# Kernel optimization log

Measured on AMD Instinct MI355X. Metric: run time of the kernel, lower is better.

Reference implementation:

```python
import jax, jax.numpy as jnp
import numpy as np

EPS = 1e-3  # BatchNorm eps in the original module


def conv3d(x, w, stride=1, pad=1):
    # x: (N,C,D,H,W), w: (O,I,3,3,3)
    return jax.lax.conv_general_dilated(
        x, w, (stride,) * 3, [(pad, pad)] * 3,
        dimension_numbers=("NCDHW", "OIDHW", "NCDHW"))


def bn_relu_mask(x, scale, shift, mask):
    # eval-mode BatchNorm folded to affine (scale/shift), ReLU, then re-mask
    # so inactive voxels stay exactly zero (submanifold semantics).
    y = jax.nn.relu(x * scale[None, :, None, None, None] + shift[None, :, None, None, None])
    return y * mask


def downsample_mask(mask):
    # output site of SparseConv3d(k=3,s=2,p=1) is active iff any active input
    # voxel lies in its receptive field -> max-pool of the mask.
    return jax.lax.reduce_window(
        mask, 0.0, jax.lax.max, (1, 1, 3, 3, 3), (1, 1, 2, 2, 2),
        [(0, 0), (0, 0), (1, 1), (1, 1), (1, 1)])


def trilinear_sample(vol, coords):
    # vol: (C,D,H,W); coords: (N,3) in [-1,1], order (x,y,z) -> (W,H,D).
    # Matches F.grid_sample(mode='bilinear', padding_mode='zeros', align_corners=True).
    C, D, H, W = vol.shape
    fx = (coords[:, 0] + 1.0) * 0.5 * (W - 1)
    fy = (coords[:, 1] + 1.0) * 0.5 * (H - 1)
    fz = (coords[:, 2] + 1.0) * 0.5 * (D - 1)
    x0 = jnp.floor(fx); y0 = jnp.floor(fy); z0 = jnp.floor(fz)
    tx = fx - x0; ty = fy - y0; tz = fz - z0
    x0i = x0.astype(jnp.int32); y0i = y0.astype(jnp.int32); z0i = z0.astype(jnp.int32)
    out = jnp.zeros((C, coords.shape[0]), vol.dtype)
    for dz in (0, 1):
        for dy in (0, 1):
            for dx in (0, 1):
                xi = x0i + dx; yi = y0i + dy; zi = z0i + dz
                w = (jnp.where(dx, tx, 1.0 - tx) * jnp.where(dy, ty, 1.0 - ty)
                     * jnp.where(dz, tz, 1.0 - tz))
                valid = ((xi >= 0) & (xi < W) & (yi >= 0) & (yi < H)
                         & (zi >= 0) & (zi < D))
                xc = jnp.clip(xi, 0, W - 1); yc = jnp.clip(yi, 0, H - 1)
                zc = jnp.clip(zi, 0, D - 1)
                vals = vol[:, zc, yc, xc]  # (C,N)
                out = out + vals * (w * valid.astype(vol.dtype))[None, :]
    return out


def setup_inputs() -> dict:
    key = jax.random.key(0)
    ks = jax.random.split(key, 24)
    D = 128
    NPTS = 65536
    x_feat = jax.random.normal(ks[0], (1, 3, D, D, D), jnp.float32)
    mask = (jax.random.uniform(ks[1], (1, 1, D, D, D)) < 0.1).astype(jnp.int32)
    coords = jax.random.uniform(ks[2], (NPTS, 3), jnp.float32, -1.0, 1.0)

    def w(k, o, i):
        return jax.random.normal(k, (o, i, 3, 3, 3), jnp.float32) * 0.05

    def bn(k, c):
        k1, k2 = jax.random.split(k)
        scale = jax.random.uniform(k1, (c,), jnp.float32, 0.5, 1.5)
        shift = jax.random.normal(k2, (c,), jnp.float32) * 0.1
        return scale, shift

    w0a = w(ks[3], 16, 3); s0a, b0a = bn(ks[4], 16)
    w0b = w(ks[5], 16, 16); s0b, b0b = bn(ks[6], 16)
    wd0 = w(ks[7], 32, 16); sd0, bd0 = bn(ks[8], 32)
    w1a = w(ks[9], 32, 32); s1a, b1a = bn(ks[10], 32)
    w1b = w(ks[11], 32, 32); s1b, b1b = bn(ks[12], 32)
    return dict(x_feat=x_feat, mask=mask, coords=coords,
                w0a=w0a, s0a=s0a, b0a=b0a, w0b=w0b, s0b=s0b, b0b=b0b,
                wd0=wd0, sd0=sd0, bd0=bd0,
                w1a=w1a, s1a=s1a, b1a=b1a, w1b=w1b, s1b=s1b, b1b=b1b)


def reference(x_feat, mask, coords, w0a, s0a, b0a, w0b, s0b, b0b,
              wd0, sd0, bd0, w1a, s1a, b1a, w1b, s1b, b1b):
    m0 = mask.astype(x_feat.dtype)
    x = x_feat * m0  # features exist only at active voxels
    # conv0: double submanifold conv (3->16->16), active set unchanged
    h = bn_relu_mask(conv3d(x, w0a), s0a, b0a, m0)
    h = bn_relu_mask(conv3d(h, w0b), s0b, b0b, m0)
    # down0: strided sparse conv 16->32, stride 2, pad 1
    m1 = downsample_mask(m0)
    h = bn_relu_mask(conv3d(h, wd0, stride=2), sd0, bd0, m1)
    # conv1: double submanifold conv 32->32 on the downsampled active set
    h = bn_relu_mask(conv3d(h, w1a), s1a, b1a, m1)
    h = bn_relu_mask(conv3d(h, w1b), s1b, b1b, m1)
    # dense + grid_sample (align_corners=True, zeros padding) -> (N, 32)
    feat = trilinear_sample(h[0], coords)  # (32, N)
    return feat.T
```

## Files before the change

kernel.cpp:

```cpp
#include <hip/hip_runtime.h>
#include <hip/hip_bf16.h>

#define N   128
#define N3  (N*N*N)
#define M   64
#define M3  (M*M*M)
#define NPTS 65536
#define PD  66
#define PD2 (PD*PD)
#define PVOX (PD*PD*PD)
#define PH  130
#define PH2 (PH*PH)
#define PH3 (PH*PH*PH)
#define CAP   393216
#define ZSLOT (CAP - 1)

enum : int {
  OW0A = 0,
  OW0B = 1296,
  OWD0 = 8208,
  OW1A = 22032,
  OW1B = 49680,
  OS0A = 77328, OB0A = 77344,
  OS0B = 77360, OB0B = 77376,
  OSD0 = 77392, OBD0 = 77424,
  OS1A = 77456, OB1A = 77488,
  OS1B = 77520, OB1B = 77552,
  WTOT = 77584
};

enum : int {
  IW0A = 0,
  IW0B = 2048,
  IWD0 = 9216,
  IW1A = 23552,
  IW1B = 51200,
  ITOT = 78848
};

typedef short bf16x8 __attribute__((ext_vector_type(8)));
typedef float f32x4  __attribute__((ext_vector_type(4)));

__device__ __forceinline__ unsigned short f2bf_bits(float f) {
  __hip_bfloat16 b = __float2bfloat16(f);
  union { __hip_bfloat16 b; unsigned short u; } cv; cv.b = b; return cv.u;
}
__device__ __forceinline__ float bfbits2f(short s) {
  union { unsigned u; float f; } c; c.u = ((unsigned)(unsigned short)s) << 16; return c.f;
}

__device__ __forceinline__ float ldIn(const void* p, long i, int bf) {
  return bf ? __bfloat162float(((const __hip_bfloat16*)p)[i]) : ((const float*)p)[i];
}

__global__ void probe_k(const unsigned* __restrict__ s0a_raw, int* __restrict__ flag) {
  if (threadIdx.x == 0 && blockIdx.x == 0) {
    int all = 1;
    for (int i = 0; i < 8; ++i) {
      unsigned w = s0a_raw[i];
      if (((w >> 8) & 0xFFu) != 0x3Fu) all = 0;
    }
    *flag = all;
  }
}

__global__ __launch_bounds__(256) void cvt_k(
    const void* w0a, const void* w0b, const void* wd0,
    const void* w1a, const void* w1b,
    const void* s0a, const void* b0a,
    const void* s0b, const void* b0b,
    const void* sd0, const void* bd0,
    const void* s1a, const void* b1a,
    const void* s1b, const void* b1b,
    const int* __restrict__ flag, float* __restrict__ wbuf)
{
  int i = blockIdx.x * 256 + threadIdx.x;
  if (i >= WTOT) return;
  int bf = *flag;
  const void* src; int off;
  if      (i < OW0B) { src = w0a; off = OW0A; }
  else if (i < OWD0) { src = w0b; off = OW0B; }
  else if (i < OW1A) { src = wd0; off = OWD0; }
  else if (i < OW1B) { src = w1a; off = OW1A; }
  else if (i < OS0A) { src = w1b; off = OW1B; }
  else if (i < OB0A) { src = s0a; off = OS0A; }
  else if (i < OS0B) { src = b0a; off = OB0A; }
  else if (i < OB0B) { src = s0b; off = OS0B; }
  else if (i < OSD0) { src = b0b; off = OB0B; }
  else if (i < OBD0) { src = sd0; off = OSD0; }
  else if (i < OS1A) { src = bd0; off = OBD0; }
  else if (i < OB1A) { src = s1a; off = OS1A; }
  else if (i < OS1B) { src = b1a; off = OB1A; }
  else if (i < OB1B) { src = s1b; off = OS1B; }
  else               { src = b1b; off = OB1B; }
  wbuf[i] = ldIn(src, i - off, bf);
}

__global__ __launch_bounds__(256) void wtrans_k(const float* __restrict__ wbuf,
                                               short* __restrict__ WI)
{
  int i = blockIdx.x * 256 + threadIdx.x;
  if (i >= 27648) return;
  if (i < 2048) {
    int kb = i >> 9, l = (i >> 3) & 63, j = i & 7;
    int k = ((l >> 4) << 3) + j;
    int tap = kb * 8 + (k >> 2), ch = k & 3, oc = l & 15;
    float v = (tap < 27 && ch < 3) ? wbuf[OW0A + (oc * 3 + ch) * 27 + tap] : 0.f;
    WI[IW0A + i] = (short)f2bf_bits(v);
  }
  if (i < 7168) {
    int p = i >> 9, l = (i >> 3) & 63, j = i & 7;
    int kg = ((l >> 4) << 3) + j;
    int tap = 2 * p + (kg >> 4);
    int ic = kg & 15, oc = l & 15;
    float v = (tap < 27) ? wbuf[OW0B + (oc * 16 + ic) * 27 + tap] : 0.f;
    WI[IW0B + i] = (short)f2bf_bits(v);
  }
  if (i < 14336) {
    int p = i >> 10, h = (i >> 9) & 1, l = (i >> 3) & 63, j = i & 7;
    int kg = ((l >> 4) << 3) + j;
    int tap = 2 * p + (kg >> 4);
    int ic = kg & 15;
    int oc = (h << 4) + (l & 15);
    float v = (tap < 27) ? wbuf[OWD0 + (oc * 16 + ic) * 27 + tap] : 0.f;
    WI[IWD0 + i] = (short)f2bf_bits(v);
  }
  {
    int t = i >> 10, h = (i >> 9) & 1, l = (i >> 3) & 63, j = i & 7;
    int ic = ((l >> 4) << 3) + j;
    int oc = (h << 4) + (l & 15);
    WI[IW1A + i] = (short)f2bf_bits(wbuf[OW1A + (oc * 32 + ic) * 27 + t]);
    WI[IW1B + i] = (short)f2bf_bits(wbuf[OW1B + (oc * 32 + ic) * 27 + t]);
  }
}

__global__ __launch_bounds__(256) void masklist_k(const int* __restrict__ mask,
                                                  int* __restrict__ list,
                                                  int* __restrict__ idxvol,
                                                  int* __restrict__ cnt)
{
  __shared__ int lpos, lbase;
  int t = threadIdx.x;
  int start = blockIdx.x * 8192;
  if (t == 0) lpos = 0;
  __syncthreads();
  int myc = 0;
  #pragma unroll 4
  for (int i = 0; i < 32; ++i) myc += (mask[start + i * 256 + t] != 0);
  atomicAdd(&lpos, myc);
  __syncthreads();
  if (t == 0) { lbase = atomicAdd(cnt, lpos); lpos = 0; }
  __syncthreads();
  #pragma unroll 4
  for (int i = 0; i < 32; ++i) {
    int idx = start + i * 256 + t;
    if (mask[idx]) {
      int p = atomicAdd(&lpos, 1);
      int slot = lbase + p;
      if (slot < ZSLOT) {
        list[slot] = idx;
        int z = idx >> 14, y = (idx >> 7) & 127, x = idx & 127;
        idxvol[((z + 1) * PH + (y + 1)) * PH + (x + 1)] = slot;
      }
    }
  }
}

__global__ __launch_bounds__(256) void dsmask_k(const int* __restrict__ mask,
                                                float* __restrict__ m1f)
{
  int idx = blockIdx.x * 256 + threadIdx.x;
  if (idx >= M3) return;
  int z = idx >> 12, y = (idx >> 6) & 63, x = idx & 63;
  int r = 0;
  #pragma unroll
  for (int dz = 0; dz < 3; ++dz) {
    int iz = 2 * z + dz - 1;
    if ((unsigned)iz >= 128u) continue;
    #pragma unroll
    for (int dy = 0; dy < 3; ++dy) {
      int iy = 2 * y + dy - 1;
      if ((unsigned)iy >= 128u) continue;
      #pragma unroll
      for (int dx = 0; dx < 3; ++dx) {
        int ix = 2 * x + dx - 1;
        if ((unsigned)ix >= 128u) continue;
        r |= mask[(iz << 14) | (iy << 7) | ix];
      }
    }
  }
  m1f[idx] = r ? 1.f : 0.f;
}

__global__ __launch_bounds__(256) void pack_c_k(const void* __restrict__ xf,
                                                const int* __restrict__ flag,
                                                const int* __restrict__ list,
                                                const int* __restrict__ cnt,
                                                short* __restrict__ xc)
{
  int nact = *cnt;
  int bf = *flag;
  for (int i = blockIdx.x * 256 + threadIdx.x; i < nact; i += 1024 * 256) {
    int idx = list[i];
    union { unsigned short us[4]; uint2 v; } u;
    u.us[0] = f2bf_bits(ldIn(xf, idx, bf));
    u.us[1] = f2bf_bits(ldIn(xf, (long)N3 + idx, bf));
    u.us[2] = f2bf_bits(ldIn(xf, 2l * N3 + idx, bf));
    u.us[3] = 0;
    *(uint2*)(xc + (size_t)i * 4) = u.v;
  }
}

__device__ __forceinline__ int tap_shift_PH(int t) {
  if (t >= 27) return 0;
  int dz = t / 9, r9 = t - dz * 9, dy = r9 / 3, dx = r9 - dy * 3;
  return (dz - 1) * PH2 + (dy - 1) * PH + (dx - 1);
}
__device__ __forceinline__ int slot_of(const int* __restrict__ idxvol, int nb) {
  int s = idxvol[nb];
  return s < 0 ? ZSLOT : s;
}

__global__ __launch_bounds__(256) void conv0a_mfma_k(
    const short* __restrict__ xc, const int* __restrict__ idxvol,
    const int* __restrict__ list, const int* __restrict__ cnt,
    const short* __restrict__ WI, const float* __restrict__ wbuf,
    short* __restrict__ h0c)
{
  __shared__ short ldsB[4 * 512];
  int tid = threadIdx.x;
  if (tid < 256) ((uint4*)ldsB)[tid] = ((const uint4*)(WI + IW0A))[tid];
  __syncthreads();
  int nact = *cnt;
  int wave = tid >> 6, lane = tid & 63, quad = lane >> 4, l15 = lane & 15;
  const int SAFE = PH2 + PH + 1;
  for (int base = blockIdx.x * 256; base < nact; base += 1024 * 256) {
    int i0 = base + wave * 64;
    int pv[4];
    #pragma unroll
    for (int tt = 0; tt < 4; ++tt) {
      int e2 = i0 + tt * 16 + l15;
      if (e2 < nact) {
        int idx = list[e2];
        int z = idx >> 14, y = (idx >> 7) & 127, x = idx & 127;
        pv[tt] = ((z + 1) * PH + (y + 1)) * PH + (x + 1);
      } else pv[tt] = SAFE;
    }
    f32x4 acc[4];
    #pragma unroll
    for (int tt = 0; tt < 4; ++tt) { f32x4 zf = {0.f,0.f,0.f,0.f}; acc[tt] = zf; }
    #pragma unroll
    for (int kb = 0; kb < 4; ++kb) {
      int t0 = kb * 8 + quad * 2, t1 = t0 + 1;
      int s0 = tap_shift_PH(t0), s1 = tap_shift_PH(t1);
      bf16x8 b = *(const bf16x8*)&ldsB[(kb * 64 + lane) * 8];
      #pragma unroll
      for (int tt = 0; tt < 4; ++tt) {
        int sa = slot_of(idxvol, pv[tt] + s0);
        int sb2 = slot_of(idxvol, pv[tt] + s1);
        union { struct { uint2 lo, hi; } p; bf16x8 v; } cv;
        cv.p.lo = *(const uint2*)(xc + (size_t)sa * 4);
        cv.p.hi = *(const uint2*)(xc + (size_t)sb2 * 4);
        acc[tt] = __builtin_amdgcn_mfma_f32_16x16x32_bf16(cv.v, b, acc[tt], 0, 0, 0);
      }
    }
    float sc = wbuf[OS0A + l15], sb = wbuf[OB0A + l15];
    #pragma unroll
    for (int tt = 0; tt < 4; ++tt)
      #pragma unroll
      for (int r = 0; r < 4; ++r) {
        int e2 = i0 + tt * 16 + quad * 4 + r;
        if (e2 < nact) {
          float vv = fmaxf(fmaf(acc[tt][r], sc, sb), 0.f);
          h0c[(size_t)e2 * 16 + l15] = (short)f2bf_bits(vv);
        }
      }
  }
}

__global__ __launch_bounds__(256) void conv0b_mfma_k(
    const short* __restrict__ h0c, const int* __restrict__ idxvol,
    const int* __restrict__ list, const int* __restrict__ cnt,
    const short* __restrict__ WI, const float* __restrict__ wbuf,
    short* __restrict__ h1c)
{
  __shared__ short ldsB[14 * 512];
  int tid = threadIdx.x;
  for (int i = tid; i < 14 * 64; i += 256)
    ((uint4*)ldsB)[i] = ((const uint4*)(WI + IW0B))[i];
  __syncthreads();
  int nact = *cnt;
  int wave = tid >> 6, lane = tid & 63, quad = lane >> 4, l15 = lane & 15;
  const int SAFE = PH2 + PH + 1;
  for (int base = blockIdx.x * 256; base < nact; base += 1024 * 256) {
    int i0 = base + wave * 64;
    int pv[4];
    #pragma unroll
    for (int tt = 0; tt < 4; ++tt) {
      int e2 = i0 + tt * 16 + l15;
      if (e2 < nact) {
        int idx = list[e2];
        int z = idx >> 14, y = (idx >> 7) & 127, x = idx & 127;
        pv[tt] = ((z + 1) * PH + (y + 1)) * PH + (x + 1);
      } else pv[tt] = SAFE;
    }
    f32x4 acc[4];
    #pragma unroll
    for (int tt = 0; tt < 4; ++tt) { f32x4 zf = {0.f,0.f,0.f,0.f}; acc[tt] = zf; }
    #pragma unroll
    for (int p = 0; p < 14; ++p) {
      const int t1 = 2 * p, t2 = (2 * p + 1 < 27) ? 2 * p + 1 : 2 * p;
      const int s1 = ((t1 / 9) - 1) * PH2 + (((t1 % 9) / 3) - 1) * PH + ((t1 % 3) - 1);
      const int s2 = ((t2 / 9) - 1) * PH2 + (((t2 % 9) / 3) - 1) * PH + ((t2 % 3) - 1);
      int sh = (quad >= 2) ? s2 : s1;
      bf16x8 b = *(const bf16x8*)&ldsB[(p * 64 + lane) * 8];
      #pragma unroll
      for (int tt = 0; tt < 4; ++tt) {
        int ss = slot_of(idxvol, pv[tt] + sh);
        bf16x8 a = *(const bf16x8*)(h0c + (size_t)ss * 16 + ((quad & 1) << 3));
        acc[tt] = __builtin_amdgcn_mfma_f32_16x16x32_bf16(a, b, acc[tt], 0, 0, 0);
      }
    }
    float sc = wbuf[OS0B + l15], sb = wbuf[OB0B + l15];
    #pragma unroll
    for (int tt = 0; tt < 4; ++tt)
      #pragma unroll
      for (int r = 0; r < 4; ++r) {
        int e2 = i0 + tt * 16 + quad * 4 + r;
        if (e2 < nact) {
          float vv = fmaxf(fmaf(acc[tt][r], sc, sb), 0.f);
          h1c[(size_t)e2 * 16 + l15] = (short)f2bf_bits(vv);
        }
      }
  }
}

__global__ __launch_bounds__(256) void convd0_mfma_k(
    const short* __restrict__ h1c, const int* __restrict__ idxvol,
    const float* __restrict__ m1f,
    const short* __restrict__ WI, const float* __restrict__ wbuf,
    short* __restrict__ Pout)
{
  __shared__ short ldsB[14 * 1024];
  int tid = threadIdx.x;
  for (int i = tid; i < 14 * 128; i += 256)
    ((uint4*)ldsB)[i] = ((const uint4*)(WI + IWD0))[i];
  __syncthreads();
  int wave = tid >> 6, lane = tid & 63, quad = lane >> 4, l15 = lane & 15;
  int rowid = blockIdx.x * 4 + wave;
  int z = rowid >> 6, y = rowid & 63;
  int base_row = ((2 * z) * PH + 2 * y) * PH;
  f32x4 acc[4][2];
  #pragma unroll
  for (int tt = 0; tt < 4; ++tt)
  #pragma unroll
  for (int h = 0; h < 2; ++h) { f32x4 zf = {0.f,0.f,0.f,0.f}; acc[tt][h] = zf; }
  #pragma unroll
  for (int p = 0; p < 14; ++p) {
    const int t1 = 2 * p, t2 = (2 * p + 1 < 27) ? 2 * p + 1 : 2 * p;
    const int s1 = (t1 / 9) * PH2 + ((t1 % 9) / 3) * PH + (t1 % 3);
    const int s2 = (t2 / 9) * PH2 + ((t2 % 9) / 3) * PH + (t2 % 3);
    int sh = (quad >= 2) ? s2 : s1;
    bf16x8 b0 = *(const bf16x8*)&ldsB[((p * 2 + 0) * 64 + lane) * 8];
    bf16x8 b1 = *(const bf16x8*)&ldsB[((p * 2 + 1) * 64 + lane) * 8];
    bf16x8 a[4];
    #pragma unroll
    for (int tt = 0; tt < 4; ++tt) {
      int vin = base_row + sh + 2 * (tt * 16 + l15);
      int ss = slot_of(idxvol, vin);
      a[tt] = *(const bf16x8*)(h1c + (size_t)ss * 16 + ((quad & 1) << 3));
    }
    #pragma unroll
    for (int tt = 0; tt < 4; ++tt) {
      acc[tt][0] = __builtin_amdgcn_mfma_f32_16x16x32_bf16(a[tt], b0, acc[tt][0], 0, 0, 0);
      acc[tt][1] = __builtin_amdgcn_mfma_f32_16x16x32_bf16(a[tt], b1, acc[tt][1], 0, 0, 0);
    }
  }
  float sc[2] = { wbuf[OSD0 + l15], wbuf[OSD0 + 16 + l15] };
  float sb[2] = { wbuf[OBD0 + l15], wbuf[OBD0 + 16 + l15] };
  int mrow = (z * 64 + y) * 64;
  int obase = ((z + 1) * PD + (y + 1)) * PD + 1;
  #pragma unroll
  for (int tt = 0; tt < 4; ++tt) {
    float4 mv = *(const float4*)&m1f[mrow + tt * 16 + quad * 4];
    float mvr[4] = {mv.x, mv.y, mv.z, mv.w};
    #pragma unroll
    for (int h = 0; h < 2; ++h)
      #pragma unroll
      for (int r = 0; r < 4; ++r) {
        float vv = fmaxf(fmaf(acc[tt][h][r], sc[h], sb[h]), 0.f) * mvr[r];
        int vox = obase + tt * 16 + quad * 4 + r;
        Pout[(size_t)vox * 32 + h * 16 + l15] = (short)f2bf_bits(vv);
      }
  }
}

__global__ __launch_bounds__(256) void conv1_mfma_k(
    const short* __restrict__ Pin, short* __restrict__ Pout,
    const short* __restrict__ WI, const float* __restrict__ wbuf,
    int sof, int bof, const float* __restrict__ m1f)
{
  __shared__ short ldsB[27 * 1024];
  int tid = threadIdx.x;
  for (int i = tid; i < 27 * 128; i += 256)
    ((uint4*)ldsB)[i] = ((const uint4*)WI)[i];
  __syncthreads();

  int wave = tid >> 6, lane = tid & 63;
  int quad = lane >> 4, l15 = lane & 15;

  f32x4 acc[2][4][2];
  #pragma unroll
  for (int rr = 0; rr < 2; ++rr)
  #pragma unroll
  for (int tt = 0; tt < 4; ++tt)
  #pragma unroll
  for (int h = 0; h < 2; ++h) {
    f32x4 zf = {0.f, 0.f, 0.f, 0.f};
    acc[rr][tt][h] = zf;
  }

  int rowid0 = blockIdx.x * 8 + wave * 2;
  int abase[2], zz[2], yy[2];
  #pragma unroll
  for (int rr = 0; rr < 2; ++rr) {
    int rowid = rowid0 + rr;
    zz[rr] = rowid >> 6; yy[rr] = rowid & 63;
    abase[rr] = ((zz[rr] + 1) * PD + (yy[rr] + 1)) * PD + 1;
  }

  #pragma unroll 1
  for (int k = 0; k < 27; ++k) {
    int dz = k / 9, r9 = k - dz * 9, dy = r9 / 3, dx = r9 - dy * 3;
    int shift = (dz - 1) * PD2 + (dy - 1) * PD + (dx - 1);
    bf16x8 b0 = *(const bf16x8*)&ldsB[((k * 2 + 0) * 64 + lane) * 8];
    bf16x8 b1 = *(const bf16x8*)&ldsB[((k * 2 + 1) * 64 + lane) * 8];
    bf16x8 a[2][4];
    #pragma unroll
    for (int rr = 0; rr < 2; ++rr)
    #pragma unroll
    for (int tt = 0; tt < 4; ++tt) {
      int off = (abase[rr] + shift + tt * 16 + l15) * 32 + quad * 8;
      a[rr][tt] = *(const bf16x8*)(Pin + off);
    }
    #pragma unroll
    for (int rr = 0; rr < 2; ++rr)
    #pragma unroll
    for (int tt = 0; tt < 4; ++tt) {
      acc[rr][tt][0] = __builtin_amdgcn_mfma_f32_16x16x32_bf16(a[rr][tt], b0, acc[rr][tt][0], 0, 0, 0);
      acc[rr][tt][1] = __builtin_amdgcn_mfma_f32_16x16x32_bf16(a[rr][tt], b1, acc[rr][tt][1], 0, 0, 0);
    }
  }

  float sc[2] = { wbuf[sof + l15], wbuf[sof + 16 + l15] };
  float sh[2] = { wbuf[bof + l15], wbuf[bof + 16 + l15] };

  #pragma unroll
  for (int rr = 0; rr < 2; ++rr) {
    int mrow = (zz[rr] * 64 + yy[rr]) * 64;
    #pragma unroll
    for (int tt = 0; tt < 4; ++tt) {
      const float4 mv = *(const float4*)&m1f[mrow + tt * 16 + quad * 4];
      float mvr[4] = {mv.x, mv.y, mv.z, mv.w};
      #pragma unroll
      for (int h = 0; h < 2; ++h) {
        #pragma unroll
        for (int r = 0; r < 4; ++r) {
          float v = fmaxf(fmaf(acc[rr][tt][h][r], sc[h], sh[h]), 0.f) * mvr[r];
          int vox = abase[rr] + tt * 16 + quad * 4 + r;
          Pout[vox * 32 + h * 16 + l15] = (short)f2bf_bits(v);
        }
      }
    }
  }
}

__global__ __launch_bounds__(256) void sample_k(
    const void* __restrict__ coords, const int* __restrict__ flag,
    const short* __restrict__ vol, void* __restrict__ out)
{
  int p = blockIdx.x * 256 + threadIdx.x;
  if (p >= NPTS) return;
  int bf = *flag;
  float cx = ldIn(coords, 3l * p + 0, bf);
  float cy = ldIn(coords, 3l * p + 1, bf);
  float cz = ldIn(coords, 3l * p + 2, bf);
  float fx = (cx + 1.f) * 0.5f * 63.f;
  float fy = (cy + 1.f) * 0.5f * 63.f;
  float fz = (cz + 1.f) * 0.5f * 63.f;
  float x0f = floorf(fx), y0f = floorf(fy), z0f = floorf(fz);
  int x0 = (int)x0f, y0 = (int)y0f, z0 = (int)z0f;
  float tx = fx - x0f, ty = fy - y0f, tz = fz - z0f;
  int li[8]; float wt[8];
  #pragma unroll
  for (int dz = 0; dz < 2; ++dz)
  #pragma unroll
  for (int dy = 0; dy < 2; ++dy)
  #pragma unroll
  for (int dx = 0; dx < 2; ++dx) {
    int t = dz * 4 + dy * 2 + dx;
    int xi = x0 + dx, yi = y0 + dy, zi = z0 + dz;
    bool ok = (unsigned)xi < 64u && (unsigned)yi < 64u && (unsigned)zi < 64u;
    int xc = min(max(xi, 0), 63), yc = min(max(yi, 0), 63), zc = min(max(zi, 0), 63);
    li[t] = ((zc + 1) * PD + (yc + 1)) * PD + (xc + 1);
    float w = (dx ? tx : 1.f - tx) * (dy ? ty : 1.f - ty) * (dz ? tz : 1.f - tz);
    wt[t] = ok ? w : 0.f;
  }
  #pragma unroll
  for (int cc = 0; cc < 4; ++cc) {
    float s[8];
    #pragma unroll
    for (int j = 0; j < 8; ++j) s[j] = 0.f;
    #pragma unroll
    for (int t = 0; t < 8; ++t) {
      bf16x8 v = *(const bf16x8*)(vol + (size_t)li[t] * 32 + cc * 8);
      #pragma unroll
      for (int j = 0; j < 8; ++j) s[j] += bfbits2f(v[j]) * wt[t];
    }
    if (bf) {
      union { unsigned short us[8]; uint4 v; } u;
      #pragma unroll
      for (int j = 0; j < 8; ++j) u.us[j] = f2bf_bits(s[j]);
      ((uint4*)out)[p * 4 + cc] = u.v;
    } else {
      #pragma unroll
      for (int j = 0; j < 8; ++j) ((float*)out)[(size_t)p * 32 + cc * 8 + j] = s[j];
    }
  }
}

extern "C" void kernel_launch(void* const* d_in, const int* in_sizes, int n_in,
                              void* d_out, int out_size, void* d_ws, size_t ws_size,
                              hipStream_t stream)
{
  const void* xf     = d_in[0];
  const int*  mask   = (const int*)d_in[1];
  const void* coords = d_in[2];
  const void* w0a = d_in[3];
  const void* s0a = d_in[4];
  const void* b0a = d_in[5];
  const void* w0b = d_in[6];
  const void* s0b = d_in[7];
  const void* b0b = d_in[8];
  const void* wd0 = d_in[9];
  const void* sd0 = d_in[10];
  const void* bd0 = d_in[11];
  const void* w1a = d_in[12];
  const void* s1a = d_in[13];
  const void* b1a = d_in[14];
  const void* w1b = d_in[15];
  const void* s1b = d_in[16];
  const void* b1b = d_in[17];

  char* ws = (char*)d_ws;
  size_t cur = 0;
  auto alloc = [&](size_t bytes) -> size_t {
    size_t o = cur; cur = (cur + bytes + 255) & ~(size_t)255; return o;
  };
  size_t o_flag = alloc(4);
  size_t o_cnt  = alloc(4);
  size_t o_m1f  = alloc((size_t)M3 * 4);
  size_t o_wbuf = alloc((size_t)WTOT * 4);
  size_t o_WI   = alloc((size_t)ITOT * 2);
  size_t o_list = alloc((size_t)CAP * 4);
  size_t o_idx  = alloc((size_t)PH3 * 4);
  size_t o_xc   = alloc((size_t)CAP * 4 * 2);
  size_t o_h0c  = alloc((size_t)CAP * 16 * 2);
  size_t o_h1c  = alloc((size_t)CAP * 16 * 2);
  size_t o_P1   = alloc((size_t)PVOX * 32 * 2);
  size_t o_P2   = alloc((size_t)PVOX * 32 * 2);

  int*   flag   = (int*)(ws + o_flag);
  int*   cnt    = (int*)(ws + o_cnt);
  float* m1f    = (float*)(ws + o_m1f);
  float* wbuf   = (float*)(ws + o_wbuf);
  short* WI     = (short*)(ws + o_WI);
  int*   list   = (int*)(ws + o_list);
  int*   idxvol = (int*)(ws + o_idx);
  short* xc     = (short*)(ws + o_xc);
  short* h0c    = (short*)(ws + o_h0c);
  short* h1c    = (short*)(ws + o_h1c);
  short* P1     = (short*)(ws + o_P1);
  short* P2     = (short*)(ws + o_P2);

  hipMemsetAsync(cnt, 0, 4, stream);
  hipMemsetAsync(idxvol, 0xFF, (size_t)PH3 * 4, stream);
  hipMemsetAsync(ws + o_xc, 0, (o_P2 - o_xc) + (size_t)PVOX * 32 * 2, stream);

  probe_k<<<1, 64, 0, stream>>>((const unsigned*)s0a, flag);
  cvt_k<<<(WTOT + 255) / 256, 256, 0, stream>>>(w0a, w0b, wd0, w1a, w1b,
                                                s0a, b0a, s0b, b0b, sd0, bd0,
                                                s1a, b1a, s1b, b1b, flag, wbuf);
  wtrans_k<<<108, 256, 0, stream>>>(wbuf, WI);
  masklist_k<<<256, 256, 0, stream>>>(mask, list, idxvol, cnt);
  dsmask_k<<<M3 / 256, 256, 0, stream>>>(mask, m1f);

  pack_c_k<<<1024, 256, 0, stream>>>(xf, flag, list, cnt, xc);
  conv0a_mfma_k<<<1024, 256, 0, stream>>>(xc, idxvol, list, cnt, WI, wbuf, h0c);
  conv0b_mfma_k<<<1024, 256, 0, stream>>>(h0c, idxvol, list, cnt, WI, wbuf, h1c);
  convd0_mfma_k<<<1024, 256, 0, stream>>>(h1c, idxvol, m1f, WI, wbuf, P1);

  conv1_mfma_k<<<512, 256, 0, stream>>>(P1, P2, WI + IW1A, wbuf, OS1A, OB1A, m1f);
  conv1_mfma_k<<<512, 256, 0, stream>>>(P2, P1, WI + IW1B, wbuf, OS1B, OB1B, m1f);

  sample_k<<<NPTS / 256, 256, 0, stream>>>(coords, flag, P1, d_out);
}
```

Baseline: 307.2 us.

## Fuse prep kernels, inline dtype detection, and pipeline conv1 A-loads

Merges the dtype probe, weight conversion and weight transpose into one prep kernel, and fuses mask listing, downsample-mask and feature packing into one kernel, cutting the launch count. conv1 now gives each wave one row instead of two and doubles the grid. It also software-pipelines the A-fragment loads across taps and shrinks LDS by keeping the last tap's weights in registers. The fewer launches and higher occupancy are meant to hide memory latency, at the cost of more register pressure and every kernel re-deriving the dtype flag.

Measured after the change: 346.6 us. +12.8%, slower.

```diff
diff --git a/kernel.cpp b/kernel.cpp
--- a/kernel.cpp
+++ b/kernel.cpp
@@ -16,20 +16,6 @@
 #define ZSLOT (CAP - 1)
 
 enum : int {
-  OW0A = 0,
-  OW0B = 1296,
-  OWD0 = 8208,
-  OW1A = 22032,
-  OW1B = 49680,
-  OS0A = 77328, OB0A = 77344,
-  OS0B = 77360, OB0B = 77376,
-  OSD0 = 77392, OBD0 = 77424,
-  OS1A = 77456, OB1A = 77488,
-  OS1B = 77520, OB1B = 77552,
-  WTOT = 77584
-};
-
-enum : int {
   IW0A = 0,
   IW0B = 2048,
   IWD0 = 9216,
@@ -38,6 +24,12 @@
   ITOT = 78848
 };
 
+enum : int {
+  SS0A = 0,   SB0A = 16,  SS0B = 32,  SB0B = 48,
+  SSD0 = 64,  SBD0 = 96,  SS1A = 128, SB1A = 160,
+  SS1B = 192, SB1B = 224, STOT = 256
+};
+
 typedef short bf16x8 __attribute__((ext_vector_type(8)));
 typedef float f32x4  __attribute__((ext_vector_type(4)));
 
@@ -48,64 +40,35 @@
 __device__ __forceinline__ float bfbits2f(short s) {
   union { unsigned u; float f; } c; c.u = ((unsigned)(unsigned short)s) << 16; return c.f;
 }
-
 __device__ __forceinline__ float ldIn(const void* p, long i, int bf) {
   return bf ? __bfloat162float(((const __hip_bfloat16*)p)[i]) : ((const float*)p)[i];
 }
-
-__global__ void probe_k(const unsigned* __restrict__ s0a_raw, int* __restrict__ flag) {
-  if (threadIdx.x == 0 && blockIdx.x == 0) {
-    int all = 1;
-    for (int i = 0; i < 8; ++i) {
-      unsigned w = s0a_raw[i];
-      if (((w >> 8) & 0xFFu) != 0x3Fu) all = 0;
-    }
-    *flag = all;
-  }
-}
-
-__global__ __launch_bounds__(256) void cvt_k(
+__device__ __forceinline__ int detect_bf(const unsigned* __restrict__ s0a_raw) {
+  int all = 1;
+  #pragma unroll
+  for (int i = 0; i < 8; ++i) {
+    unsigned w = s0a_raw[i];
+    if (((w >> 8) & 0xFFu) != 0x3Fu) all = 0;
+  }
+  return all;
+}
+
+__global__ __launch_bounds__(256) void prep_k(
     const void* w0a, const void* w0b, const void* wd0,
     const void* w1a, const void* w1b,
-    const void* s0a, const void* b0a,
-    const void* s0b, const void* b0b,
-    const void* sd0, const void* bd0,
-    const void* s1a, const void* b1a,
+    const void* s0a, const void* b0a, const void* s0b, const void* b0b,
+    const void* sd0, const void* bd0, const void* s1a, const void* b1a,
     const void* s1b, const void* b1b,
-    const int* __restrict__ flag, float* __restrict__ wbuf)
+    short* __restrict__ WI, float* __restrict__ sbuf)
 {
   int i = blockIdx.x * 256 + threadIdx.x;
-  if (i >= WTOT) return;
-  int bf = *flag;
-  const void* src; int off;
-  if      (i < OW0B) { src = w0a; off = OW0A; }
-  else if (i < OWD0) { src = w0b; off = OW0B; }
-  else if (i < OW1A) { src = wd0; off = OWD0; }
-  else if (i < OW1B) { src = w1a; off = OW1A; }
-  else if (i < OS0A) { src = w1b; off = OW1B; }
-  else if (i < OB0A) { src = s0a; off = OS0A; }
-  else if (i < OS0B) { src = b0a; off = OB0A; }
-  else if (i < OB0B) { src = s0b; off = OS0B; }
-  else if (i < OSD0) { src = b0b; off = OB0B; }
-  else if (i < OBD0) { src = sd0; off = OSD0; }
-  else if (i < OS1A) { src = bd0; off = OBD0; }
-  else if (i < OB1A) { src = s1a; off = OS1A; }
-  else if (i < OS1B) { src = b1a; off = OB1A; }
-  else if (i < OB1B) { src = s1b; off = OS1B; }
-  else               { src = b1b; off = OB1B; }
-  wbuf[i] = ldIn(src, i - off, bf);
-}
-
-__global__ __launch_bounds__(256) void wtrans_k(const float* __restrict__ wbuf,
-                                               short* __restrict__ WI)
-{
-  int i = blockIdx.x * 256 + threadIdx.x;
-  if (i >= 27648) return;
+  if (i >= 27648 + STOT) return;
+  int bf = detect_bf((const unsigned*)s0a);
   if (i < 2048) {
     int kb = i >> 9, l = (i >> 3) & 63, j = i & 7;
     int k = ((l >> 4) << 3) + j;
     int tap = kb * 8 + (k >> 2), ch = k & 3, oc = l & 15;
-    float v = (tap < 27 && ch < 3) ? wbuf[OW0A + (oc * 3 + ch) * 27 + tap] : 0.f;
+    float v = (tap < 27 && ch < 3) ? ldIn(w0a, (oc * 3 + ch) * 27 + tap, bf) : 0.f;
     WI[IW0A + i] = (short)f2bf_bits(v);
   }
   if (i < 7168) {
@@ -113,7 +76,7 @@
     int kg = ((l >> 4) << 3) + j;
     int tap = 2 * p + (kg >> 4);
     int ic = kg & 15, oc = l & 15;
-    float v = (tap < 27) ? wbuf[OW0B + (oc * 16 + ic) * 27 + tap] : 0.f;
+    float v = (tap < 27) ? ldIn(w0b, (oc * 16 + ic) * 27 + tap, bf) : 0.f;
     WI[IW0B + i] = (short)f2bf_bits(v);
   }
   if (i < 14336) {
@@ -122,24 +85,64 @@
     int tap = 2 * p + (kg >> 4);
     int ic = kg & 15;
     int oc = (h << 4) + (l & 15);
-    float v = (tap < 27) ? wbuf[OWD0 + (oc * 16 + ic) * 27 + tap] : 0.f;
+    float v = (tap < 27) ? ldIn(wd0, (oc * 16 + ic) * 27 + tap, bf) : 0.f;
     WI[IWD0 + i] = (short)f2bf_bits(v);
   }
-  {
+  if (i < 27648) {
     int t = i >> 10, h = (i >> 9) & 1, l = (i >> 3) & 63, j = i & 7;
     int ic = ((l >> 4) << 3) + j;
     int oc = (h << 4) + (l & 15);
-    WI[IW1A + i] = (short)f2bf_bits(wbuf[OW1A + (oc * 32 + ic) * 27 + t]);
-    WI[IW1B + i] = (short)f2bf_bits(wbuf[OW1B + (oc * 32 + ic) * 27 + t]);
-  }
-}
-
-__global__ __launch_bounds__(256) void masklist_k(const int* __restrict__ mask,
-                                                  int* __restrict__ list,
-                                                  int* __restrict__ idxvol,
-                                                  int* __restrict__ cnt)
-{
+    WI[IW1A + i] = (short)f2bf_bits(ldIn(w1a, (oc * 32 + ic) * 27 + t, bf));
+    WI[IW1B + i] = (short)f2bf_bits(ldIn(w1b, (oc * 32 + ic) * 27 + t, bf));
+  } else {
+    int j = i - 27648;
+    const void* src; int loc;
+    if      (j < 16)  { src = s0a; loc = j; }
+    else if (j < 32)  { src = b0a; loc = j - 16; }
+    else if (j < 48)  { src = s0b; loc = j - 32; }
+    else if (j < 64)  { src = b0b; loc = j - 48; }
+    else if (j < 96)  { src = sd0; loc = j - 64; }
+    else if (j < 128) { src = bd0; loc = j - 96; }
+    else if (j < 160) { src = s1a; loc = j - 128; }
+    else if (j < 192) { src = b1a; loc = j - 160; }
+    else if (j < 224) { src = s1b; loc = j - 192; }
+    else              { src = b1b; loc = j - 224; }
+    sbuf[j] = ldIn(src, loc, bf);
+  }
+}
+
+__global__ __launch_bounds__(256) void maskprep_k(
+    const int* __restrict__ mask, const void* __restrict__ xf,
+    const void* __restrict__ s0a,
+    int* __restrict__ list, int* __restrict__ idxvol, int* __restrict__ cnt,
+    float* __restrict__ m1f, short* __restrict__ xc)
+{
+  if (blockIdx.x >= 256) {
+    int idx = (blockIdx.x - 256) * 256 + threadIdx.x;
+    if (idx >= M3) return;
+    int z = idx >> 12, y = (idx >> 6) & 63, x = idx & 63;
+    int r = 0;
+    #pragma unroll
+    for (int dz = 0; dz < 3; ++dz) {
+      int iz = 2 * z + dz - 1;
+      if ((unsigned)iz >= 128u) continue;
+      #pragma unroll
+      for (int dy = 0; dy < 3; ++dy) {
+        int iy = 2 * y + dy - 1;
+        if ((unsigned)iy >= 128u) continue;
+        #pragma unroll
+        for (int dx = 0; dx < 3; ++dx) {
+          int ix = 2 * x + dx - 1;
+          if ((unsigned)ix >= 128u) continue;
+          r |= mask[(iz << 14) | (iy << 7) | ix];
+        }
+      }
+    }
+    m1f[idx] = r ? 1.f : 0.f;
+    return;
+  }
   __shared__ int lpos, lbase;
+  int bf = detect_bf((const unsigned*)s0a);
   int t = threadIdx.x;
   int start = blockIdx.x * 8192;
   if (t == 0) lpos = 0;
@@ -161,53 +164,14 @@
         list[slot] = idx;
         int z = idx >> 14, y = (idx >> 7) & 127, x = idx & 127;
         idxvol[((z + 1) * PH + (y + 1)) * PH + (x + 1)] = slot;
-      }
-    }
-  }
-}
-
-__global__ __launch_bounds__(256) void dsmask_k(const int* __restrict__ mask,
-                                                float* __restrict__ m1f)
-{
-  int idx = blockIdx.x * 256 + threadIdx.x;
-  if (idx >= M3) return;
-  int z = idx >> 12, y = (idx >> 6) & 63, x = idx & 63;
-  int r = 0;
-  #pragma unroll
-  for (int dz = 0; dz < 3; ++dz) {
-    int iz = 2 * z + dz - 1;
-    if ((unsigned)iz >= 128u) continue;
-    #pragma unroll
-    for (int dy = 0; dy < 3; ++dy) {
-      int iy = 2 * y + dy - 1;
-      if ((unsigned)iy >= 128u) continue;
-      #pragma unroll
-      for (int dx = 0; dx < 3; ++dx) {
-        int ix = 2 * x + dx - 1;
-        if ((unsigned)ix >= 128u) continue;
-        r |= mask[(iz << 14) | (iy << 7) | ix];
-      }
-    }
-  }
-  m1f[idx] = r ? 1.f : 0.f;
-}
-
-__global__ __launch_bounds__(256) void pack_c_k(const void* __restrict__ xf,
-                                                const int* __restrict__ flag,
-                                                const int* __restrict__ list,
-                                                const int* __restrict__ cnt,
-                                                short* __restrict__ xc)
-{
-  int nact = *cnt;
-  int bf = *flag;
-  for (int i = blockIdx.x * 256 + threadIdx.x; i < nact; i += 1024 * 256) {
-    int idx = list[i];
-    union { unsigned short us[4]; uint2 v; } u;
-    u.us[0] = f2bf_bits(ldIn(xf, idx, bf));
-    u.us[1] = f2bf_bits(ldIn(xf, (long)N3 + idx, bf));
-    u.us[2] = f2bf_bits(ldIn(xf, 2l * N3 + idx, bf));
-    u.us[3] = 0;
-    *(uint2*)(xc + (size_t)i * 4) = u.v;
+        union { unsigned short us[4]; uint2 v; } u;
+        u.us[0] = f2bf_bits(ldIn(xf, idx, bf));
+        u.us[1] = f2bf_bits(ldIn(xf, (long)N3 + idx, bf));
+        u.us[2] = f2bf_bits(ldIn(xf, 2l * N3 + idx, bf));
+        u.us[3] = 0;
+        *(uint2*)(xc + (size_t)slot * 4) = u.v;
+      }
+    }
   }
 }
 
@@ -224,7 +188,7 @@
 __global__ __launch_bounds__(256) void conv0a_mfma_k(
     const short* __restrict__ xc, const int* __restrict__ idxvol,
     const int* __restrict__ list, const int* __restrict__ cnt,
-    const short* __restrict__ WI, const float* __restrict__ wbuf,
+    const short* __restrict__ WI, const float* __restrict__ sbuf,
     short* __restrict__ h0c)
 {
   __shared__ short ldsB[4 * 512];
@@ -264,7 +228,7 @@
         acc[tt] = __builtin_amdgcn_mfma_f32_16x16x32_bf16(cv.v, b, acc[tt], 0, 0, 0);
       }
     }
-    float sc = wbuf[OS0A + l15], sb = wbuf[OB0A + l15];
+    float sc = sbuf[SS0A + l15], sb = sbuf[SB0A + l15];
     #pragma unroll
     for (int tt = 0; tt < 4; ++tt)
       #pragma unroll
@@ -281,7 +245,7 @@
 __global__ __launch_bounds__(256) void conv0b_mfma_k(
     const short* __restrict__ h0c, const int* __restrict__ idxvol,
     const int* __restrict__ list, const int* __restrict__ cnt,
-    const short* __restrict__ WI, const float* __restrict__ wbuf,
+    const short* __restrict__ WI, const float* __restrict__ sbuf,
     short* __restrict__ h1c)
 {
   __shared__ short ldsB[14 * 512];
@@ -321,7 +285,7 @@
         acc[tt] = __builtin_amdgcn_mfma_f32_16x16x32_bf16(a, b, acc[tt], 0, 0, 0);
       }
     }
-    float sc = wbuf[OS0B + l15], sb = wbuf[OB0B + l15];
+    float sc = sbuf[SS0B + l15], sb = sbuf[SB0B + l15];
     #pragma unroll
     for (int tt = 0; tt < 4; ++tt)
       #pragma unroll
@@ -338,7 +302,7 @@
 __global__ __launch_bounds__(256) void convd0_mfma_k(
     const short* __restrict__ h1c, const int* __restrict__ idxvol,
     const float* __restrict__ m1f,
-    const short* __restrict__ WI, const float* __restrict__ wbuf,
+    const short* __restrict__ WI, const float* __restrict__ sbuf,
     short* __restrict__ Pout)
 {
   __shared__ short ldsB[14 * 1024];
@@ -376,8 +340,8 @@
       acc[tt][1] = __builtin_amdgcn_mfma_f32_16x16x32_bf16(a[tt], b1, acc[tt][1], 0, 0, 0);
     }
   }
-  float sc[2] = { wbuf[OSD0 + l15], wbuf[OSD0 + 16 + l15] };
-  float sb[2] = { wbuf[OBD0 + l15], wbuf[OBD0 + 16 + l15] };
+  float sc[2] = { sbuf[SSD0 + l15], sbuf[SSD0 + 16 + l15] };
+  float sb[2] = { sbuf[SBD0 + l15], sbuf[SBD0 + 16 + l15] };
   int mrow = (z * 64 + y) * 64;
   int obase = ((z + 1) * PD + (y + 1)) * PD + 1;
   #pragma unroll
@@ -397,91 +361,99 @@
 
 __global__ __launch_bounds__(256) void conv1_mfma_k(
     const short* __restrict__ Pin, short* __restrict__ Pout,
-    const short* __restrict__ WI, const float* __restrict__ wbuf,
+    const short* __restrict__ WI, const float* __restrict__ sbuf,
     int sof, int bof, const float* __restrict__ m1f)
 {
-  __shared__ short ldsB[27 * 1024];
+  __shared__ short ldsB[26 * 1024];
   int tid = threadIdx.x;
-  for (int i = tid; i < 27 * 128; i += 256)
+  for (int i = tid; i < 26 * 128; i += 256)
     ((uint4*)ldsB)[i] = ((const uint4*)WI)[i];
-  __syncthreads();
 
   int wave = tid >> 6, lane = tid & 63;
   int quad = lane >> 4, l15 = lane & 15;
 
-  f32x4 acc[2][4][2];
-  #pragma unroll
-  for (int rr = 0; rr < 2; ++rr)
+  bf16x8 b26[2];
+  b26[0] = *(const bf16x8*)(WI + 26 * 1024 + 0 * 512 + lane * 8);
+  b26[1] = *(const bf16x8*)(WI + 26 * 1024 + 1 * 512 + lane * 8);
+  __syncthreads();
+
+  f32x4 acc[4][2];
   #pragma unroll
   for (int tt = 0; tt < 4; ++tt)
   #pragma unroll
-  for (int h = 0; h < 2; ++h) {
-    f32x4 zf = {0.f, 0.f, 0.f, 0.f};
-    acc[rr][tt][h] = zf;
-  }
-
-  int rowid0 = blockIdx.x * 8 + wave * 2;
-  int abase[2], zz[2], yy[2];
-  #pragma unroll
-  for (int rr = 0; rr < 2; ++rr) {
-    int rowid = rowid0 + rr;
-    zz[rr] = rowid >> 6; yy[rr] = rowid & 63;
-    abase[rr] = ((zz[rr] + 1) * PD + (yy[rr] + 1)) * PD + 1;
-  }
-
+  for (int h = 0; h < 2; ++h) { f32x4 zf = {0.f,0.f,0.f,0.f}; acc[tt][h] = zf; }
+
+  int rowid = blockIdx.x * 4 + wave;
+  int zz = rowid >> 6, yy = rowid & 63;
+  int abase = ((zz + 1) * PD + (yy + 1)) * PD + 1;
+
+  bf16x8 a_cur[4];
+  {
+    const int shift0 = -PD2 - PD - 1;
+    #pragma unroll
+    for (int tt = 0; tt < 4; ++tt) {
+      int off = (abase + shift0 + tt * 16 + l15) * 32 + quad * 8;
+      a_cur[tt] = *(const bf16x8*)(Pin + off);
+    }
+  }
   #pragma unroll 1
   for (int k = 0; k < 27; ++k) {
-    int dz = k / 9, r9 = k - dz * 9, dy = r9 / 3, dx = r9 - dy * 3;
-    int shift = (dz - 1) * PD2 + (dy - 1) * PD + (dx - 1);
-    bf16x8 b0 = *(const bf16x8*)&ldsB[((k * 2 + 0) * 64 + lane) * 8];
-    bf16x8 b1 = *(const bf16x8*)&ldsB[((k * 2 + 1) * 64 + lane) * 8];
-    bf16x8 a[2][4];
-    #pragma unroll
-    for (int rr = 0; rr < 2; ++rr)
+    bf16x8 a_nxt[4];
+    if (k < 26) {
+      int kk = k + 1;
+      int dz = kk / 9, r9 = kk - dz * 9, dy = r9 / 3, dx = r9 - dy * 3;
+      int shift = (dz - 1) * PD2 + (dy - 1) * PD + (dx - 1);
+      #pragma unroll
+      for (int tt = 0; tt < 4; ++tt) {
+        int off = (abase + shift + tt * 16 + l15) * 32 + quad * 8;
+        a_nxt[tt] = *(const bf16x8*)(Pin + off);
+      }
+    }
+    bf16x8 b0, b1;
+    if (k < 26) {
+      b0 = *(const bf16x8*)&ldsB[((k * 2 + 0) * 64 + lane) * 8];
+      b1 = *(const bf16x8*)&ldsB[((k * 2 + 1) * 64 + lane) * 8];
+    } else {
+      b0 = b26[0]; b1 = b26[1];
+    }
     #pragma unroll
     for (int tt = 0; tt < 4; ++tt) {
-      int off = (abase[rr] + shift + tt * 16 + l15) * 32 + quad * 8;
-      a[rr][tt] = *(const bf16x8*)(Pin + off);
-    }
-    #pragma unroll
-    for (int rr = 0; rr < 2; ++rr)
-    #pragma unroll
-    for (int tt = 0; tt < 4; ++tt) {
-      acc[rr][tt][0] = __builtin_amdgcn_mfma_f32_16x16x32_bf16(a[rr][tt], b0, acc[rr][tt][0], 0, 0, 0);
-      acc[rr][tt][1] = __builtin_amdgcn_mfma_f32_16x16x32_bf16(a[rr][tt], b1, acc[rr][tt][1], 0, 0, 0);
-    }
-  }
-
-  float sc[2] = { wbuf[sof + l15], wbuf[sof + 16 + l15] };
-  float sh[2] = { wbuf[bof + l15], wbuf[bof + 16 + l15] };
-
-  #pragma unroll
-  for (int rr = 0; rr < 2; ++rr) {
-    int mrow = (zz[rr] * 64 + yy[rr]) * 64;
-    #pragma unroll
-    for (int tt = 0; tt < 4; ++tt) {
-      const float4 mv = *(const float4*)&m1f[mrow + tt * 16 + quad * 4];
-      float mvr[4] = {mv.x, mv.y, mv.z, mv.w};
-      #pragma unroll
-      for (int h = 0; h < 2; ++h) {
-        #pragma unroll
-        for (int r = 0; r < 4; ++r) {
-          float v = fmaxf(fmaf(acc[rr][tt][h][r], sc[h], sh[h]), 0.f) * mvr[r];
-          int vox = abase[rr] + tt * 16 + quad * 4 + r;
-          Pout[vox * 32 + h * 16 + l15] = (short)f2bf_bits(v);
-        }
+      acc[tt][0] = __builtin_amdgcn_mfma_f32_16x16x32_bf16(a_cur[tt], b0, acc[tt][0], 0, 0, 0);
+      acc[tt][1] = __builtin_amdgcn_mfma_f32_16x16x32_bf16(a_cur[tt], b1, acc[tt][1], 0, 0, 0);
+    }
+    if (k < 26) {
+      #pragma unroll
+      for (int tt = 0; tt < 4; ++tt) a_cur[tt] = a_nxt[tt];
+    }
+  }
+
+  float sc[2] = { sbuf[sof + l15], sbuf[sof + 16 + l15] };
+  float sh[2] = { sbuf[bof + l15], sbuf[bof + 16 + l15] };
+
+  int mrow = (zz * 64 + yy) * 64;
+  #pragma unroll
+  for (int tt = 0; tt < 4; ++tt) {
+    const float4 mv = *(const float4*)&m1f[mrow + tt * 16 + quad * 4];
+    float mvr[4] = {mv.x, mv.y, mv.z, mv.w};
+    #pragma unroll
+    for (int h = 0; h < 2; ++h) {
+      #pragma unroll
+      for (int r = 0; r < 4; ++r) {
+        float v = fmaxf(fmaf(acc[tt][h][r], sc[h], sh[h]), 0.f) * mvr[r];
+        int vox = abase + tt * 16 + quad * 4 + r;
+        Pout[(size_t)vox * 32 + h * 16 + l15] = (short)f2bf_bits(v);
       }
     }
   }
 }
 
 __global__ __launch_bounds__(256) void sample_k(
-    const void* __restrict__ coords, const int* __restrict__ flag,
+    const void* __restrict__ coords, const void* __restrict__ s0a,
     const short* __restrict__ vol, void* __restrict__ out)
 {
   int p = blockIdx.x * 256 + threadIdx.x;
   if (p >= NPTS) return;
-  int bf = *flag;
+  int bf = detect_bf((const unsigned*)s0a);
   float cx = ldIn(coords, 3l * p + 0, bf);
   float cy = ldIn(coords, 3l * p + 1, bf);
   float cz = ldIn(coords, 3l * p + 2, bf);
@@ -557,10 +529,9 @@
   auto alloc = [&](size_t bytes) -> size_t {
     size_t o = cur; cur = (cur + bytes + 255) & ~(size_t)255; return o;
   };
-  size_t o_flag = alloc(4);
   size_t o_cnt  = alloc(4);
   size_t o_m1f  = alloc((size_t)M3 * 4);
-  size_t o_wbuf = alloc((size_t)WTOT * 4);
+  size_t o_sbuf = alloc((size_t)STOT * 4);
   size_t o_WI   = alloc((size_t)ITOT * 2);
   size_t o_list = alloc((size_t)CAP * 4);
   size_t o_idx  = alloc((size_t)PH3 * 4);
@@ -570,10 +541,9 @@
   size_t o_P1   = alloc((size_t)PVOX * 32 * 2);
   size_t o_P2   = alloc((size_t)PVOX * 32 * 2);
 
-  int*   flag   = (int*)(ws + o_flag);
   int*   cnt    = (int*)(ws + o_cnt);
   float* m1f    = (float*)(ws + o_m1f);
-  float* wbuf   = (float*)(ws + o_wbuf);
+  float* sbuf   = (float*)(ws + o_sbuf);
   short* WI     = (short*)(ws + o_WI);
   int*   list   = (int*)(ws + o_list);
   int*   idxvol = (int*)(ws + o_idx);
@@ -587,21 +557,18 @@
   hipMemsetAsync(idxvol, 0xFF, (size_t)PH3 * 4, stream);
   hipMemsetAsync(ws + o_xc, 0, (o_P2 - o_xc) + (size_t)PVOX * 32 * 2, stream);
 
-  probe_k<<<1, 64, 0, stream>>>((const unsigned*)s0a, flag);
-  cvt_k<<<(WTOT + 255) / 256, 256, 0, stream>>>(w0a, w0b, wd0, w1a, w1b,
-                                                s0a, b0a, s0b, b0b, sd0, bd0,
-                                                s1a, b1a, s1b, b1b, flag, wbuf);
-  wtrans_k<<<108, 256, 0, stream>>>(wbuf, WI);
-  masklist_k<<<256, 256, 0, stream>>>(mask, list, idxvol, cnt);
-  dsmask_k<<<M3 / 256, 256, 0, stream>>>(mask, m1f);
-
-  pack_c_k<<<1024, 256, 0, stream>>>(xf, flag, list, cnt, xc);
-  conv0a_mfma_k<<<1024, 256, 0, stream>>>(xc, idxvol, list, cnt, WI, wbuf, h0c);
-  conv0b_mfma_k<<<1024, 256, 0, stream>>>(h0c, idxvol, list, cnt, WI, wbuf, h1c);
-  convd0_mfma_k<<<1024, 256, 0, stream>>>(h1c, idxvol, m1f, WI, wbuf, P1);
-
-  conv1_mfma_k<<<512, 256, 0, stream>>>(P1, P2, WI + IW1A, wbuf, OS1A, OB1A, m1f);
-  conv1_mfma_k<<<512, 256, 0, stream>>>(P2, P1, WI + IW1B, wbuf, OS1B, OB1B, m1f);
-
-  sample_k<<<NPTS / 256, 256, 0, stream>>>(coords, flag, P1, d_out);
-}
+  prep_k<<<(27648 + STOT + 255) / 256, 256, 0, stream>>>(
+      w0a, w0b, wd0, w1a, w1b,
+      s0a, b0a, s0b, b0b, sd0, bd0, s1a, b1a, s1b, b1b, WI, sbuf);
+  maskprep_k<<<256 + M3 / 256, 256, 0, stream>>>(mask, xf, s0a, list, idxvol,
+                                                 cnt, m1f, xc);
+
+  conv0a_mfma_k<<<1024, 256, 0, stream>>>(xc, idxvol, list, cnt, WI, sbuf, h0c);
+  conv0b_mfma_k<<<1024, 256, 0, stream>>>(h0c, idxvol, list, cnt, WI, sbuf, h1c);
+  convd0_mfma_k<<<1024, 256, 0, stream>>>(h1c, idxvol, m1f, WI, sbuf, P1);
+
+  conv1_mfma_k<<<1024, 256, 0, stream>>>(P1, P2, WI + IW1A, sbuf, SS1A, SB1A, m1f);
+  conv1_mfma_k<<<1024, 256, 0, stream>>>(P2, P1, WI + IW1B, sbuf, SS1B, SB1B, m1f);
+
+  sample_k<<<NPTS / 256, 256, 0, stream>>>(coords, s0a, P1, d_out);
+}
```
